# Optimization experiments

Hardware: AMD Instinct MI355X
Metric: run time of the kernel (lower is better)

## Reference

```python
import jax, jax.numpy as jnp
import numpy as np

TOP_K = 4

def setup_inputs() -> dict:
    key = jax.random.key(0)
    ks = jax.random.split(key, 10)
    s = 0.02
    return {
        "x": jax.random.normal(ks[0], (4, 1024, 2048), jnp.float32),
        "expert_bias": jnp.zeros((64,), jnp.float32),
        "router_w": jax.random.normal(ks[1], (64, 2048), jnp.float32) * s,
        "gate_w": jax.random.normal(ks[2], (8192, 2048), jnp.float32) * s,
        "up_w": jax.random.normal(ks[3], (8192, 2048), jnp.float32) * s,
        "down_w": jax.random.normal(ks[4], (2048, 8192), jnp.float32) * s,
        "w_down": jax.random.normal(ks[5], (512, 2048), jnp.float32) * s,
        "w_up": jax.random.normal(ks[6], (2048, 512), jnp.float32) * s,
        "experts_w12": jax.random.normal(ks[7], (64, 512, 2048), jnp.float32) * s,
        "experts_w3": jax.random.normal(ks[8], (64, 1024, 512), jnp.float32) * s,
    }


def reference(x, expert_bias, router_w, gate_w, up_w, down_w, w_down, w_up, experts_w12, experts_w3):
    B, S, D = x.shape
    E = router_w.shape[0]
    K = TOP_K
    h = x.reshape(-1, D)            # [N, D]
    N = h.shape[0]
    NK = N * K

    # --- router (fp32) ---
    logits = h @ router_w.T          # [N, E]
    scores = jax.nn.sigmoid(logits)
    z_loss = jnp.mean(logits * logits) * 1e-4
    sel = scores + expert_bias
    _, topk_idx = jax.lax.top_k(sel, K)                      # [N, K]
    topk_logits = jnp.take_along_axis(logits, topk_idx, axis=1)
    gating = jax.nn.softmax(topk_logits, axis=-1)            # [N, K]

    # --- shared SwiGLU expert ---
    shared = (jax.nn.silu(h @ gate_w.T) * (h @ up_w.T)) @ down_w.T   # [N, D]

    # --- bottleneck down projection ---
    hd = h @ w_down.T                # [N, bottle]
    Bn = hd.shape[1]

    # --- dispatch: sort tokens by expert, capacity max_load per expert ---
    flat = topk_idx.reshape(-1)                      # [NK]
    perm = jnp.argsort(flat)                         # stable sort
    sorted_e = flat[perm]
    counts = jnp.bincount(flat, length=E)
    ptr = jnp.cumsum(counts) - counts                # start offset per expert
    local = jnp.arange(NK) - ptr[sorted_e]           # rank within expert
    max_load = (NK // E // 8 + 6) * 8                # static python int
    num_slots = E * max_load
    mask = local < max_load
    slots = sorted_e * max_load + local
    tok = jnp.repeat(jnp.arange(N), K)               # token id per routed slot

    # reverse_map[slot] = token index (N = dummy)
    rm = jnp.full((num_slots + 1,), N, dtype=jnp.int32)
    rm = rm.at[jnp.where(mask, slots, num_slots)].set(tok[perm].astype(jnp.int32))
    reverse_map = rm[:num_slots]

    hwd = jnp.concatenate([hd, jnp.zeros((1, Bn), hd.dtype)], axis=0)
    padding = hwd[reverse_map].reshape(E, max_load, Bn)

    # --- grouped expert GEMMs ---
    h12 = jnp.einsum('emb,ebf->emf', padding, experts_w12)   # [E, L, 2*F]
    h1, h2 = jnp.split(h12, 2, axis=-1)
    pout = jnp.einsum('emf,efb->emb', jax.nn.silu(h1) * h2, experts_w3)
    pout = pout.reshape(-1, Bn)                              # [num_slots, bottle]

    # --- combine: gather back per (token, k) slot and mix with gating ---
    powd = jnp.concatenate([pout, jnp.zeros((1, Bn), pout.dtype)], axis=0)
    gm = jnp.full((NK + 1,), num_slots, dtype=jnp.int32)
    gm = gm.at[jnp.where(mask, perm, NK)].set(jnp.where(mask, slots, num_slots).astype(jnp.int32))
    gather_map = gm[:NK]
    gathered = powd[gather_map].reshape(N, K, Bn)
    routed_b = jnp.einsum('nk,nkb->nb', gating, gathered)
    routed = routed_b @ w_up.T                               # [N, D]

    # eval mode: route_scale = 1.0, moe_scale = 0.5 (one shared expert), aux_loss = 0
    out = (shared + routed) * 0.5
    return out.reshape(B, S, D), z_loss
```

## Files before the change

### kernel.cpp

```cpp
#include <hip/hip_runtime.h>
#include <math.h>

#define NTOK 4096
#define DMODEL 2048
#define ENUM 64
#define HSH 8192
#define BND 512
#define FEXP 1024
#define MAXL 304
#define EPAD 384
#define ECH 16

typedef float f32x4 __attribute__((ext_vector_type(4)));
using bf16x8 = __attribute__((ext_vector_type(8))) __bf16;

typedef const __attribute__((address_space(1))) unsigned int cgu32;
typedef __attribute__((address_space(3))) unsigned int lu32;
#define GLOAD16(g, l) __builtin_amdgcn_global_load_lds((cgu32*)(g), (lu32*)(l), 16, 0, 0)

__device__ __forceinline__ unsigned short f2bf(float f) {
    union { float f; unsigned int u; } v; v.f = f;
    unsigned int u = v.u;
    return (unsigned short)((u + 0x7FFFu + ((u >> 16) & 1u)) >> 16);
}
__device__ __forceinline__ float bf2f(unsigned short s) {
    union { unsigned int u; float f; } v; v.u = ((unsigned int)s) << 16;
    return v.f;
}

__global__ __launch_bounds__(256) void init_kernel(float* zacc, int* slot2tok, unsigned short* hdz) {
    int i = blockIdx.x * 256 + threadIdx.x;
    if (i == 0) *zacc = 0.f;
    if (i < ENUM * MAXL) slot2tok[i] = NTOK;
    if (i < BND) hdz[i] = 0;
}

__global__ __launch_bounds__(256) void convert_kernel(
    const float* __restrict__ in, unsigned short* __restrict__ out, long long n)
{
    long long stride = (long long)gridDim.x * 256 * 8;
    for (long long i = ((long long)blockIdx.x * 256 + threadIdx.x) * 8; i < n; i += stride) {
        float4 a = *(const float4*)(in + i);
        float4 b = *(const float4*)(in + i + 4);
        union { unsigned short s[8]; uint4 v; } o;
        o.s[0] = f2bf(a.x); o.s[1] = f2bf(a.y); o.s[2] = f2bf(a.z); o.s[3] = f2bf(a.w);
        o.s[4] = f2bf(b.x); o.s[5] = f2bf(b.y); o.s[6] = f2bf(b.z); o.s[7] = f2bf(b.w);
        *(uint4*)(out + i) = o.v;
    }
}

__global__ __launch_bounds__(256) void convert_x_kernel(
    const float* __restrict__ in, unsigned short* __restrict__ hi,
    unsigned short* __restrict__ lo, long long n)
{
    long long stride = (long long)gridDim.x * 256 * 8;
    for (long long i = ((long long)blockIdx.x * 256 + threadIdx.x) * 8; i < n; i += stride) {
        float4 a = *(const float4*)(in + i);
        float4 b = *(const float4*)(in + i + 4);
        union { unsigned short s[8]; uint4 v; } oh, ol;
        float f[8] = {a.x, a.y, a.z, a.w, b.x, b.y, b.z, b.w};
#pragma unroll
        for (int j = 0; j < 8; j++) {
            unsigned short h = f2bf(f[j]);
            oh.s[j] = h;
            ol.s[j] = f2bf(f[j] - bf2f(h));
        }
        *(uint4*)(hi + i) = oh.v;
        *(uint4*)(lo + i) = ol.v;
    }
}

__global__ __launch_bounds__(256) void convert_rw_kernel(
    const float* __restrict__ rw, unsigned short* __restrict__ whi,
    unsigned short* __restrict__ wlo)
{
    int i = (blockIdx.x * 256 + threadIdx.x) * 4;
    if (i >= 128 * 2048) return;
    ushort4 oh = {0, 0, 0, 0}, ol = {0, 0, 0, 0};
    if (i < 64 * 2048) {
        float4 f = *(const float4*)(rw + i);
        float v[4] = {f.x, f.y, f.z, f.w};
        unsigned short h;
        h = f2bf(v[0]); oh.x = h; ol.x = f2bf(v[0] - bf2f(h));
        h = f2bf(v[1]); oh.y = h; ol.y = f2bf(v[1] - bf2f(h));
        h = f2bf(v[2]); oh.z = h; ol.z = f2bf(v[2] - bf2f(h));
        h = f2bf(v[3]); oh.w = h; ol.w = f2bf(v[3] - bf2f(h));
    }
    *(ushort4*)(whi + i) = oh;
    *(ushort4*)(wlo + i) = ol;
}

__global__ __launch_bounds__(256) void tconv_kernel(
    const float* __restrict__ in, unsigned short* __restrict__ out, int Kd, int Nd)
{
    __shared__ float t[32][33];
    size_t zoff = (size_t)blockIdx.z * Kd * Nd;
    in += zoff; out += zoff;
    int n0 = blockIdx.x * 32, k0 = blockIdx.y * 32;
    int r = threadIdx.x >> 3, c = (threadIdx.x & 7) * 4;
    float4 v = *(const float4*)(in + (size_t)(k0 + r) * Nd + n0 + c);
    t[r][c] = v.x; t[r][c + 1] = v.y; t[r][c + 2] = v.z; t[r][c + 3] = v.w;
    __syncthreads();
    ushort4 o;
    o.x = f2bf(t[c + 0][r]); o.y = f2bf(t[c + 1][r]);
    o.z = f2bf(t[c + 2][r]); o.w = f2bf(t[c + 3][r]);
    *(ushort4*)(out + (size_t)(n0 + r) * Kd + k0 + c) = o;
}

__global__ __launch_bounds__(256) void rgemm_kernel(
    const unsigned short* __restrict__ xb, const unsigned short* __restrict__ xlo,
    const unsigned short* __restrict__ whi, const unsigned short* __restrict__ wlo,
    float* __restrict__ logits)
{
    __shared__ unsigned short As[2][128 * 64];
    __shared__ unsigned short Bs[2][128 * 64];
    const int z = blockIdx.z;
    const int m0 = blockIdx.y * 128;
    const int tid = threadIdx.x;
    const int lane = tid & 63;
    const int w = tid >> 6;
    const int wm = (w >> 1) * 64;
    const int wn = (w & 1) * 64;

    const unsigned short* Ab = (z == 2) ? xlo : xb;
    const unsigned short* Bb = (z == 1) ? wlo : whi;
    float* Cb = logits + (size_t)z * NTOK * 128;

    size_t asrc[4], bsrc[4];
    int ldso[4];
#pragma unroll
    for (int i = 0; i < 4; i++) {
        int u = i * 256 + tid;
        int r = u >> 3;
        int ce = ((u & 7) ^ (r & 7)) * 8;
        ldso[i] = u * 8;
        asrc[i] = (size_t)(m0 + r) * DMODEL + ce;
        bsrc[i] = (size_t)r * DMODEL + ce;
    }

    const int lrow = lane & 15;
    const int kg = lane >> 4;
    const int mk = (lrow & 7) << 4;
    int arx[4], brx[4];
#pragma unroll
    for (int t = 0; t < 4; t++) {
        arx[t] = (wm + t * 16 + lrow) * 128;
        brx[t] = (wn + t * 16 + lrow) * 128;
    }

    f32x4 acc[4][4];
#pragma unroll
    for (int a = 0; a < 4; a++)
#pragma unroll
        for (int b = 0; b < 4; b++) acc[a][b] = (f32x4)0.f;

#pragma unroll
    for (int i = 0; i < 4; i++) GLOAD16(Ab + asrc[i], &As[0][ldso[i]]);
#pragma unroll
    for (int i = 0; i < 4; i++) GLOAD16(Bb + bsrc[i], &Bs[0][ldso[i]]);
#pragma unroll
    for (int i = 0; i < 4; i++) GLOAD16(Ab + asrc[i] + 64, &As[1][ldso[i]]);
#pragma unroll
    for (int i = 0; i < 4; i++) GLOAD16(Bb + bsrc[i] + 64, &Bs[1][ldso[i]]);

    const int nt = DMODEL >> 6;
    int cur = 0;
    for (int t = 0; t < nt; ++t) {
        if (t + 1 < nt) asm volatile("s_waitcnt vmcnt(8)" ::: "memory");
        else            asm volatile("s_waitcnt vmcnt(0)" ::: "memory");
        __builtin_amdgcn_s_barrier();
        __builtin_amdgcn_sched_barrier(0);
        const char* Abase = (const char*)&As[cur][0];
        const char* Bbase = (const char*)&Bs[cur][0];
#pragma unroll
        for (int ks = 0; ks < 2; ks++) {
            const int cb = (ks * 64 + kg * 16) ^ mk;
            bf16x8 a[4], b[4];
#pragma unroll
            for (int t2 = 0; t2 < 4; t2++) {
                a[t2] = *(const bf16x8*)(Abase + arx[t2] + cb);
                b[t2] = *(const bf16x8*)(Bbase + brx[t2] + cb);
            }
#pragma unroll
            for (int ni = 0; ni < 4; ni++)
#pragma unroll
                for (int mi = 0; mi < 4; mi++)
                    acc[mi][ni] = __builtin_amdgcn_mfma_f32_16x16x32_bf16(a[mi], b[ni], acc[mi][ni], 0, 0, 0);
        }
        __builtin_amdgcn_sched_barrier(0);
        asm volatile("s_waitcnt lgkmcnt(0)" ::: "memory");
        __builtin_amdgcn_s_barrier();
        __builtin_amdgcn_sched_barrier(0);
        const int kn = (t + 2) * 64;
        if (kn < DMODEL) {
#pragma unroll
            for (int i = 0; i < 4; i++) GLOAD16(Ab + asrc[i] + kn, &As[cur][ldso[i]]);
#pragma unroll
            for (int i = 0; i < 4; i++) GLOAD16(Bb + bsrc[i] + kn, &Bs[cur][ldso[i]]);
        }
        cur ^= 1;
    }

    const int rb0 = m0 + wm + (kg << 2);
#pragma unroll
    for (int mi = 0; mi < 4; mi++)
#pragma unroll
        for (int ni = 0; ni < 4; ni++) {
            int col = wn + ni * 16 + lrow;
#pragma unroll
            for (int r = 0; r < 4; r++)
                Cb[(size_t)(rb0 + mi * 16 + r) * 128 + col] = acc[mi][ni][r];
        }
}

__global__ __launch_bounds__(256) void topk_kernel(
    const float* __restrict__ logits, const float* __restrict__ bias,
    int* __restrict__ topk_idx, float* __restrict__ gating, float* __restrict__ zacc)
{
    __shared__ float zpart[4];
    const size_t Z = (size_t)NTOK * 128;
    int wv = threadIdx.x >> 6, lane = threadIdx.x & 63;
    int n = blockIdx.x * 4 + wv;
    const float* lp = logits + (size_t)n * 128 + lane;
    float logit = lp[0] + lp[Z] + lp[2 * Z];
    float sel = 1.f / (1.f + expf(-logit)) + bias[lane];
    float zsq = logit * logit;
    for (int off = 32; off; off >>= 1) zsq += __shfl_down(zsq, off);
    if (lane == 0) zpart[wv] = zsq;
    __syncthreads();
    if (threadIdx.x == 0) atomicAdd(zacc, zpart[0] + zpart[1] + zpart[2] + zpart[3]);
    float cur = sel;
    float ch_logit[4]; int ch_idx[4];
    for (int kk = 0; kk < 4; kk++) {
        float v = cur; int idx = lane;
        for (int off = 1; off < 64; off <<= 1) {
            float v2 = __shfl_xor(v, off);
            int i2 = __shfl_xor(idx, off);
            if (v2 > v || (v2 == v && i2 < idx)) { v = v2; idx = i2; }
        }
        ch_idx[kk] = idx;
        ch_logit[kk] = __shfl(logit, idx);
        if (lane == idx) cur = -1e30f;
    }
    if (lane == 0) {
        float mx = ch_logit[0];
        for (int kk = 1; kk < 4; kk++) mx = fmaxf(mx, ch_logit[kk]);
        float se = 0.f, ex[4];
        for (int kk = 0; kk < 4; kk++) { ex[kk] = expf(ch_logit[kk] - mx); se += ex[kk]; }
        for (int kk = 0; kk < 4; kk++) {
            topk_idx[n * 4 + kk] = ch_idx[kk];
            gating[n * 4 + kk] = ex[kk] / se;
        }
    }
}

__global__ __launch_bounds__(256) void rank_kernel(
    const int* __restrict__ topk_idx, int* __restrict__ slot2tok, int* __restrict__ gmap)
{
    int e = blockIdx.x;
    __shared__ int wsum[4];
    int tid = threadIdx.x;
    int lane = tid & 63, w = tid >> 6;
    int running = 0;
    for (int c = 0; c < NTOK * 4; c += 256) {
        int i = c + tid;
        int fl = topk_idx[i];
        bool m = (fl == e);
        unsigned long long bal = __ballot(m);
        int prefix = __popcll(bal & ((1ULL << lane) - 1ULL));
        if (lane == 0) wsum[w] = __popcll(bal);
        __syncthreads();
        int wbase = 0;
        for (int j = 0; j < w; j++) wbase += wsum[j];
        int total = wsum[0] + wsum[1] + wsum[2] + wsum[3];
        if (m) {
            int rank = running + wbase + prefix;
            int tok = i >> 2;
            if (rank < MAXL) {
                slot2tok[e * MAXL + rank] = tok;
                gmap[i] = e * MAXL + rank;
            } else gmap[i] = -1;
        }
        running += total;
        __syncthreads();
    }
}

template<int GATHER, int EPI>
__global__ __launch_bounds__(256) void gemm2(
    const unsigned short* __restrict__ A, long long aZ, int lda,
    const int* __restrict__ gtab,
    const unsigned short* __restrict__ Bm, long long bZ, int ldb,
    void* __restrict__ Cb, long long cZ, int ldc,
    int M, int K)
{
    __shared__ unsigned short As[2][128 * 64];
    __shared__ unsigned short Bs[2][128 * 64];
    const int z = blockIdx.z;
    const int m0 = blockIdx.y * 128;
    const int n0 = blockIdx.x * 128;
    const int tid = threadIdx.x;
    const int lane = tid & 63;
    const int w = tid >> 6;
    const int wm = (w >> 1) * 64;
    const int wn = (w & 1) * 64;

    const unsigned short* Ab = A + (GATHER ? (size_t)0 : (size_t)z * aZ);
    const unsigned short* Bb = Bm + (size_t)z * bZ;

    size_t asrc[4], bsrc[4];
    int ldso[4];
#pragma unroll
    for (int i = 0; i < 4; i++) {
        int u = i * 256 + tid;
        int r = u >> 3;
        int ce = ((u & 7) ^ (r & 7)) * 8;
        ldso[i] = u * 8;
        if constexpr (GATHER) {
            int mr = m0 + r;
            int tok = (mr < M) ? gtab[(size_t)z * MAXL + mr] : NTOK;
            asrc[i] = (size_t)tok * lda + ce;
        } else {
            asrc[i] = (size_t)(m0 + r) * lda + ce;
        }
        bsrc[i] = (size_t)(n0 + r) * ldb + ce;
    }

    const int lrow = lane & 15;
    const int kg = lane >> 4;
    const int mk = (lrow & 7) << 4;
    int arx[4], brx[4];
#pragma unroll
    for (int t = 0; t < 4; t++) {
        arx[t] = (wm + t * 16 + lrow) * 128;
        brx[t] = (wn + t * 16 + lrow) * 128;
    }

    f32x4 acc[4][4];
#pragma unroll
    for (int a = 0; a < 4; a++)
#pragma unroll
        for (int b = 0; b < 4; b++) acc[a][b] = (f32x4)0.f;

#pragma unroll
    for (int i = 0; i < 4; i++) GLOAD16(Ab + asrc[i], &As[0][ldso[i]]);
#pragma unroll
    for (int i = 0; i < 4; i++) GLOAD16(Bb + bsrc[i], &Bs[0][ldso[i]]);
    if (64 < K) {
#pragma unroll
        for (int i = 0; i < 4; i++) GLOAD16(Ab + asrc[i] + 64, &As[1][ldso[i]]);
#pragma unroll
        for (int i = 0; i < 4; i++) GLOAD16(Bb + bsrc[i] + 64, &Bs[1][ldso[i]]);
    }

    const int nt = K >> 6;
    int cur = 0;
    for (int t = 0; t < nt; ++t) {
        if (t + 1 < nt) asm volatile("s_waitcnt vmcnt(8)" ::: "memory");
        else            asm volatile("s_waitcnt vmcnt(0)" ::: "memory");
        __builtin_amdgcn_s_barrier();
        __builtin_amdgcn_sched_barrier(0);
        const char* Abase = (const char*)&As[cur][0];
        const char* Bbase = (const char*)&Bs[cur][0];
#pragma unroll
        for (int ks = 0; ks < 2; ks++) {
            const int cb = (ks * 64 + kg * 16) ^ mk;
            bf16x8 a[4], b[4];
#pragma unroll
            for (int t2 = 0; t2 < 4; t2++) {
                a[t2] = *(const bf16x8*)(Abase + arx[t2] + cb);
                b[t2] = *(const bf16x8*)(Bbase + brx[t2] + cb);
            }
#pragma unroll
            for (int ni = 0; ni < 4; ni++)
#pragma unroll
                for (int mi = 0; mi < 4; mi++)
                    acc[mi][ni] = __builtin_amdgcn_mfma_f32_16x16x32_bf16(a[mi], b[ni], acc[mi][ni], 0, 0, 0);
        }
        __builtin_amdgcn_sched_barrier(0);
        asm volatile("s_waitcnt lgkmcnt(0)" ::: "memory");
        __builtin_amdgcn_s_barrier();
        __builtin_amdgcn_sched_barrier(0);
        const int kn = (t + 2) * 64;
        if (kn < K) {
#pragma unroll
            for (int i = 0; i < 4; i++) GLOAD16(Ab + asrc[i] + kn, &As[cur][ldso[i]]);
#pragma unroll
            for (int i = 0; i < 4; i++) GLOAD16(Bb + bsrc[i] + kn, &Bs[cur][ldso[i]]);
        }
        cur ^= 1;
    }

    const int rb0 = m0 + wm + (kg << 2);
#pragma unroll
    for (int mi = 0; mi < 4; mi++)
#pragma unroll
        for (int ni = 0; ni < 4; ni++) {
            int col = n0 + wn + ni * 16 + lrow;
#pragma unroll
            for (int r = 0; r < 4; r++) {
                int row = rb0 + mi * 16 + r;
                if (row < M) {
                    size_t ci = (size_t)z * cZ + (size_t)row * ldc + col;
                    float v = acc[mi][ni][r];
                    if constexpr (EPI == 0) {
                        ((unsigned short*)Cb)[ci] = f2bf(v);
                    } else if constexpr (EPI == 1) {
                        unsigned short* cp = (unsigned short*)Cb + ci;
                        float g = bf2f(*cp);
                        *cp = f2bf(g / (1.f + expf(-g)) * v);
                    } else if constexpr (EPI == 2) {
                        ((float*)Cb)[ci] = v;
                    } else {
                        float* cp = (float*)Cb + ci;
                        *cp = (*cp + v) * 0.5f;
                    }
                }
            }
        }
}

template<int DUAL>
__global__ __launch_bounds__(512) void gemm6(
    const unsigned short* __restrict__ A, int lda,
    const unsigned short* __restrict__ B1, const unsigned short* __restrict__ B2, int ldb,
    void* __restrict__ Cb, int ldc, int ncol0, int K)
{
    constexpr int RING = DUAL ? 3 : 4;
    __shared__ unsigned short As[RING * 128 * 32];
    __shared__ unsigned short B1s[RING * 256 * 32];
    __shared__ unsigned short B2s[DUAL ? RING * 256 * 32 : 64];
    const int m0 = blockIdx.y * 128;
    const int n0 = blockIdx.x * 256;
    const int tid = threadIdx.x;
    const int lane = tid & 63;
    const int w = tid >> 6;
    const int wm = (w >> 2) * 64;
    const int wn = (w & 3) * 64;

    size_t asrc;
    int ldsoA;
    {
        int r = tid >> 2;
        int ce = ((tid & 3) ^ ((r >> 1) & 3)) * 8;
        ldsoA = tid * 8;
        asrc = (size_t)(m0 + r) * lda + ce;
    }
    size_t bsrc[2];
    int ldsoB[2];
#pragma unroll
    for (int i = 0; i < 2; i++) {
        int u = i * 512 + tid;
        int r = u >> 2;
        int ce = ((u & 3) ^ ((r >> 1) & 3)) * 8;
        ldsoB[i] = u * 8;
        bsrc[i] = (size_t)(n0 + r) * ldb + ce;
    }

    const int lrow = lane & 15;
    const int kg = lane >> 4;
    const int un = (kg ^ ((lrow >> 1) & 3)) << 4;
    int arx[4], brx[4];
#pragma unroll
    for (int mi = 0; mi < 4; mi++) arx[mi] = (wm + mi * 16 + lrow) * 64 + un;
#pragma unroll
    for (int ni = 0; ni < 4; ni++) brx[ni] = (wn + ni * 16 + lrow) * 64 + un;

    f32x4 acc1[4][4];
    f32x4 acc2[DUAL ? 4 : 1][DUAL ? 4 : 1];
#pragma unroll
    for (int a = 0; a < 4; a++)
#pragma unroll
        for (int b = 0; b < 4; b++) {
            acc1[a][b] = (f32x4)0.f;
            if constexpr (DUAL) acc2[a][b] = (f32x4)0.f;
        }

    const int NT = K >> 5;
    const int PRO = DUAL ? 2 : 3;
    for (int t = 0; t < PRO && t < NT; ++t) {
        const int kn = t * 32;
        unsigned short* as = &As[(t % RING) * 128 * 32];
        unsigned short* b1s = &B1s[(t % RING) * 256 * 32];
        GLOAD16(A + asrc + kn, &as[ldsoA]);
        GLOAD16(B1 + bsrc[0] + kn, &b1s[ldsoB[0]]);
        GLOAD16(B1 + bsrc[1] + kn, &b1s[ldsoB[1]]);
        if constexpr (DUAL) {
            unsigned short* b2s = &B2s[(t % RING) * 256 * 32];
            GLOAD16(B2 + bsrc[0] + kn, &b2s[ldsoB[0]]);
            GLOAD16(B2 + bsrc[1] + kn, &b2s[ldsoB[1]]);
        }
    }

    for (int kt = 0; kt < NT; ++kt) {
        if constexpr (DUAL) {
            if (kt + 1 < NT) asm volatile("s_waitcnt vmcnt(5)" ::: "memory");
            else             asm volatile("s_waitcnt vmcnt(0)" ::: "memory");
        } else {
            if (kt + 2 < NT)       asm volatile("s_waitcnt vmcnt(6)" ::: "memory");
            else if (kt + 1 < NT)  asm volatile("s_waitcnt vmcnt(3)" ::: "memory");
            else                   asm volatile("s_waitcnt vmcnt(0)" ::: "memory");
        }
        __builtin_amdgcn_s_barrier();
        __builtin_amdgcn_sched_barrier(0);

        const int slot = kt % RING;
        const char* Ab = (const char*)&As[slot * 128 * 32];
        const char* Bb1 = (const char*)&B1s[slot * 256 * 32];
        const char* Bb2 = DUAL ? (const char*)&B2s[slot * 256 * 32] : nullptr;

        const int tstage = kt + (DUAL ? 2 : 3);
        const bool pf = (tstage < NT);
        const int sslot = tstage % RING;
        const int kn = tstage * 32;
        unsigned short* sas = &As[sslot * 128 * 32];
        unsigned short* sb1 = &B1s[sslot * 256 * 32];
        unsigned short* sb2 = DUAL ? &B2s[sslot * 256 * 32] : nullptr;

        bf16x8 b1[4], b2[DUAL ? 4 : 1];
#pragma unroll
        for (int ni = 0; ni < 4; ni++) {
            b1[ni] = *(const bf16x8*)(Bb1 + brx[ni]);
            if constexpr (DUAL) b2[ni] = *(const bf16x8*)(Bb2 + brx[ni]);
        }

#define G6_PHASE(q, GL)                                                              \
        {                                                                            \
            bf16x8 af = *(const bf16x8*)(Ab + arx[q]);                               \
            GL;                                                                      \
            __builtin_amdgcn_s_setprio(1);                                           \
            _Pragma("unroll")                                                        \
            for (int ni = 0; ni < 4; ni++) {                                         \
                acc1[q][ni] = __builtin_amdgcn_mfma_f32_16x16x32_bf16(               \
                    af, b1[ni], acc1[q][ni], 0, 0, 0);                               \
                if constexpr (DUAL)                                                  \
                    acc2[q][ni] = __builtin_amdgcn_mfma_f32_16x16x32_bf16(           \
                        af, b2[ni], acc2[q][ni], 0, 0, 0);                           \
            }                                                                        \
            __builtin_amdgcn_s_setprio(0);                                           \
            __builtin_amdgcn_sched_barrier(0);                                       \
        }

        G6_PHASE(0, if (pf) GLOAD16(A + asrc + kn, &sas[ldsoA]))
        G6_PHASE(1, if (pf) GLOAD16(B1 + bsrc[0] + kn, &sb1[ldsoB[0]]))
        G6_PHASE(2, if (pf) { GLOAD16(B1 + bsrc[1] + kn, &sb1[ldsoB[1]]);
                              if constexpr (DUAL) GLOAD16(B2 + bsrc[0] + kn, &sb2[ldsoB[0]]); })
        G6_PHASE(3, if (pf) { if constexpr (DUAL) GLOAD16(B2 + bsrc[1] + kn, &sb2[ldsoB[1]]); })
#undef G6_PHASE
    }

    const int rb0 = m0 + wm + (kg << 2);
#pragma unroll
    for (int mi = 0; mi < 4; mi++)
#pragma unroll
        for (int ni = 0; ni < 4; ni++) {
            int col = ncol0 + n0 + wn + ni * 16 + lrow;
#pragma unroll
            for (int r = 0; r < 4; r++) {
                int row = rb0 + mi * 16 + r;
                if constexpr (DUAL) {
                    float g = acc1[mi][ni][r];
                    float u = acc2[mi][ni][r];
                    ((unsigned short*)Cb)[(size_t)row * ldc + col] =
                        f2bf(g / (1.f + expf(-g)) * u);
                } else {
                    ((float*)Cb)[(size_t)row * ldc + col] = acc1[mi][ni][r];
                }
            }
        }
}

template<int EPI>
__global__ __launch_bounds__(512) void gemm7(
    const unsigned short* __restrict__ A, int lda,
    const unsigned short* __restrict__ Bm, int ldb,
    unsigned short* __restrict__ C, int ldc, int K)
{
    __shared__ unsigned short As[2][256 * 64];
    __shared__ unsigned short Bs[2][256 * 64];
    const int m0 = blockIdx.y * 256;
    const int n0 = blockIdx.x * 256;
    const int tid = threadIdx.x;
    const int lane = tid & 63;
    const int w = tid >> 6;
    const int wm = (w >> 2) * 128;
    const int wn = (w & 3) * 64;

    size_t asrc[4], bsrc[4];
    int ldso[4];
#pragma unroll
    for (int i = 0; i < 4; i++) {
        int u = i * 512 + tid;
        int r = u >> 3;
        int ce = ((u & 7) ^ (r & 7)) * 8;
        ldso[i] = u * 8;
        asrc[i] = (size_t)(m0 + r) * lda + ce;
        bsrc[i] = (size_t)(n0 + r) * ldb + ce;
    }

    const int lrow = lane & 15;
    const int kg = lane >> 4;
    const int mk = (lrow & 7) << 4;
    int arx[8], brx[4];
#pragma unroll
    for (int mi = 0; mi < 8; mi++) arx[mi] = (wm + mi * 16 + lrow) * 128;
#pragma unroll
    for (int ni = 0; ni < 4; ni++) brx[ni] = (wn + ni * 16 + lrow) * 128;

    f32x4 acc[8][4];
#pragma unroll
    for (int a = 0; a < 8; a++)
#pragma unroll
        for (int b = 0; b < 4; b++) acc[a][b] = (f32x4)0.f;

#pragma unroll
    for (int i = 0; i < 4; i++) GLOAD16(A + asrc[i], &As[0][ldso[i]]);
#pragma unroll
    for (int i = 0; i < 4; i++) GLOAD16(Bm + bsrc[i], &Bs[0][ldso[i]]);

    const int NT = K >> 6;
    for (int t = 0; t < NT; ++t) {
        asm volatile("s_waitcnt vmcnt(0)" ::: "memory");
        __builtin_amdgcn_s_barrier();
        __builtin_amdgcn_sched_barrier(0);

        const char* Ab = (const char*)&As[t & 1][0];
        const char* Bb = (const char*)&Bs[t & 1][0];
        const bool pf = (t + 1 < NT);
        const int nb = (t + 1) & 1;
        const int kn = (t + 1) * 64;
        const int cb0 = (kg * 16) ^ mk;
        const int cb1 = (64 + kg * 16) ^ mk;

        bf16x8 b0[4], b1v[4];
        bf16x8 af[4];

#define G7_PHASE(MH, KS, CB, READB, GL0, GL1)                                        \
        {                                                                            \
            if constexpr (READB) {                                                   \
                _Pragma("unroll")                                                    \
                for (int ni = 0; ni < 4; ni++)                                       \
                    ((KS) ? b1v : b0)[ni] = *(const bf16x8*)(Bb + brx[ni] + (CB));   \
            }                                                                        \
            _Pragma("unroll")                                                        \
            for (int mi = 0; mi < 4; mi++)                                           \
                af[mi] = *(const bf16x8*)(Ab + arx[(MH) * 4 + mi] + (CB));           \
            if (pf) { GL0; GL1; }                                                    \
            __builtin_amdgcn_s_barrier();                                            \
            asm volatile("s_waitcnt lgkmcnt(0)" ::: "memory");                       \
            __builtin_amdgcn_sched_barrier(0);                                       \
            __builtin_amdgcn_s_setprio(1);                                           \
            _Pragma("unroll")                                                        \
            for (int ni = 0; ni < 4; ni++)                                           \
                _Pragma("unroll")                                                    \
                for (int mi = 0; mi < 4; mi++)                                       \
                    acc[(MH) * 4 + mi][ni] = __builtin_amdgcn_mfma_f32_16x16x32_bf16(\
                        af[mi], ((KS) ? b1v : b0)[ni], acc[(MH) * 4 + mi][ni], 0, 0, 0);\
            __builtin_amdgcn_s_setprio(0);                                           \
            __builtin_amdgcn_sched_barrier(0);                                       \
            __builtin_amdgcn_s_barrier();                                            \
        }

        G7_PHASE(0, 0, cb0, true,
                 GLOAD16(A + asrc[0] + kn, &As[nb][ldso[0]]),
                 GLOAD16(A + asrc[1] + kn, &As[nb][ldso[1]]))
        G7_PHASE(1, 0, cb0, false,
                 GLOAD16(A + asrc[2] + kn, &As[nb][ldso[2]]),
                 GLOAD16(A + asrc[3] + kn, &As[nb][ldso[3]]))
        G7_PHASE(0, 1, cb1, true,
                 GLOAD16(Bm + bsrc[0] + kn, &Bs[nb][ldso[0]]),
                 GLOAD16(Bm + bsrc[1] + kn, &Bs[nb][ldso[1]]))
        G7_PHASE(1, 1, cb1, false,
                 GLOAD16(Bm + bsrc[2] + kn, &Bs[nb][ldso[2]]),
                 GLOAD16(Bm + bsrc[3] + kn, &Bs[nb][ldso[3]]))
#undef G7_PHASE
    }

    const int rb0 = m0 + wm + (kg << 2);
#pragma unroll
    for (int mi = 0; mi < 8; mi++)
#pragma unroll
        for (int ni = 0; ni < 4; ni++) {
            int col = n0 + wn + ni * 16 + lrow;
#pragma unroll
            for (int r = 0; r < 4; r++) {
                int row = rb0 + mi * 16 + r;
                size_t ci = (size_t)row * ldc + col;
                float v = acc[mi][ni][r];
                if constexpr (EPI == 0) {
                    C[ci] = f2bf(v);
                } else {
                    unsigned short* cp = C + ci;
                    float g = bf2f(*cp);
                    *cp = f2bf(g / (1.f + expf(-g)) * v);
                }
            }
        }
}

__global__ __launch_bounds__(256) void siluact_kernel(
    const unsigned short* __restrict__ h12, unsigned short* __restrict__ act)
{
    int e = blockIdx.y, m = blockIdx.x;
    const unsigned short* hr = h12 + ((size_t)e * EPAD + m) * 2048;
    unsigned short* ar = act + ((size_t)e * EPAD + m) * 1024;
    int j = threadIdx.x * 4;
    ushort4 h1 = *(const ushort4*)(hr + j);
    ushort4 h2 = *(const ushort4*)(hr + 1024 + j);
    ushort4 o;
    float v;
    v = bf2f(h1.x); o.x = f2bf(v / (1.f + expf(-v)) * bf2f(h2.x));
    v = bf2f(h1.y); o.y = f2bf(v / (1.f + expf(-v)) * bf2f(h2.y));
    v = bf2f(h1.z); o.z = f2bf(v / (1.f + expf(-v)) * bf2f(h2.z));
    v = bf2f(h1.w); o.w = f2bf(v / (1.f + expf(-v)) * bf2f(h2.w));
    *(ushort4*)(ar + j) = o;
}

__global__ __launch_bounds__(256) void gather_kernel(
    const unsigned short* __restrict__ pout, const int* __restrict__ gmap,
    const float* __restrict__ gating, unsigned short* __restrict__ routed_b)
{
    int n = blockIdx.x;
    int j = threadIdx.x * 2;
    float a0 = 0.f, a1 = 0.f;
#pragma unroll
    for (int kk = 0; kk < 4; kk++) {
        int slot = gmap[n * 4 + kk];
        float g = gating[n * 4 + kk];
        if (slot >= 0) {
            const unsigned short* pr = pout + (size_t)slot * BND + j;
            a0 += g * bf2f(pr[0]);
            a1 += g * bf2f(pr[1]);
        }
    }
    routed_b[(size_t)n * BND + j] = f2bf(a0);
    routed_b[(size_t)n * BND + j + 1] = f2bf(a1);
}

__global__ void zloss_kernel(const float* zacc, float* out) {
    out[0] = zacc[0] * (1.0e-4f / (float)(NTOK * ENUM));
}

extern "C" void kernel_launch(void* const* d_in, const int* in_sizes, int n_in,
                              void* d_out, int out_size, void* d_ws, size_t ws_size,
                              hipStream_t stream)
{
    const float* x      = (const float*)d_in[0];
    const float* ebias  = (const float*)d_in[1];
    const float* rw     = (const float*)d_in[2];
    const float* gate_w = (const float*)d_in[3];
    const float* up_w   = (const float*)d_in[4];
    const float* down_w = (const float*)d_in[5];
    const float* w_down = (const float*)d_in[6];
    const float* w_up   = (const float*)d_in[7];
    const float* w12    = (const float*)d_in[8];
    const float* w3     = (const float*)d_in[9];
    float* out = (float*)d_out;

    char* ws = (char*)d_ws;
    size_t off = 0;
    auto alloc = [&](size_t b) { size_t o = off; off += (b + 255) & ~(size_t)255; return o; };
    float* zacc     = (float*)(ws + alloc(4));
    int*   topk     = (int*)(ws + alloc((size_t)NTOK * 4 * 4));
    float* gating   = (float*)(ws + alloc((size_t)NTOK * 4 * 4));
    int*   gmap     = (int*)(ws + alloc((size_t)NTOK * 4 * 4));
    int*   slot2tok = (int*)(ws + alloc((size_t)ENUM * MAXL * 4));
    unsigned short* xb     = (unsigned short*)(ws + alloc((size_t)NTOK * DMODEL * 2));
    unsigned short* hd     = (unsigned short*)(ws + alloc((size_t)(NTOK + 1) * BND * 2));
    unsigned short* rb     = (unsigned short*)(ws + alloc((size_t)NTOK * BND * 2));
    unsigned short* wdownb = (unsigned short*)(ws + alloc((size_t)BND * DMODEL * 2));
    unsigned short* wupb   = (unsigned short*)(ws + alloc((size_t)DMODEL * BND * 2));
    unsigned short* wbuf   = (unsigned short*)(ws + alloc((size_t)HSH * DMODEL * 2));
    unsigned short* H1     = (unsigned short*)(ws + alloc((size_t)NTOK * HSH * 2));
    unsigned short* h12  = H1;
    unsigned short* act  = H1 + (size_t)ECH * EPAD * 2048;
    unsigned short* pout = H1 + (size_t)ECH * EPAD * 2048 + (size_t)ECH * EPAD * 1024;
    unsigned short* xlo    = H1;
    float*          logits = (float*)((char*)H1 + (size_t)NTOK * DMODEL * 2);
    unsigned short* whi    = (unsigned short*)((char*)logits + (size_t)3 * NTOK * 128 * 4);
    unsigned short* wlo    = whi + (size_t)128 * DMODEL;

    init_kernel<<<(ENUM * MAXL + 255) / 256, 256, 0, stream>>>(zacc, slot2tok, hd + (size_t)NTOK * BND);

    convert_x_kernel<<<1024, 256, 0, stream>>>(x, xb, xlo, (long long)NTOK * DMODEL);
    convert_rw_kernel<<<(128 * 2048 / 4 + 255) / 256, 256, 0, stream>>>(rw, whi, wlo);
    rgemm_kernel<<<dim3(1, NTOK / 128, 3), 256, 0, stream>>>(xb, xlo, whi, wlo, logits);
    topk_kernel<<<NTOK / 4, 256, 0, stream>>>(logits, ebias, topk, gating, zacc);
    rank_kernel<<<ENUM, 256, 0, stream>>>(topk, slot2tok, gmap);

    convert_kernel<<<256, 256, 0, stream>>>(w_down, wdownb, (long long)BND * DMODEL);
    convert_kernel<<<256, 256, 0, stream>>>(w_up, wupb, (long long)DMODEL * BND);

    gemm2<0, 0><<<dim3(BND / 128, NTOK / 128, 1), 256, 0, stream>>>(
        xb, 0, DMODEL, nullptr, wdownb, 0, DMODEL, hd, 0, BND, NTOK, DMODEL);

    convert_kernel<<<1024, 256, 0, stream>>>(gate_w, wbuf, (long long)HSH * DMODEL);
    gemm7<0><<<dim3(HSH / 256, NTOK / 256), 512, 0, stream>>>(
        xb, DMODEL, wbuf, DMODEL, H1, HSH, DMODEL);
    convert_kernel<<<1024, 256, 0, stream>>>(up_w, wbuf, (long long)HSH * DMODEL);
    gemm7<1><<<dim3(HSH / 256, NTOK / 256), 512, 0, stream>>>(
        xb, DMODEL, wbuf, DMODEL, H1, HSH, DMODEL);
    convert_kernel<<<1024, 256, 0, stream>>>(down_w, wbuf, (long long)DMODEL * HSH);
    gemm6<0><<<dim3(DMODEL / 256, NTOK / 128), 512, 0, stream>>>(
        H1, HSH, wbuf, nullptr, HSH, out, DMODEL, 0, HSH);

    for (int c = 0; c < ENUM / ECH; c++) {
        tconv_kernel<<<dim3(2048 / 32, 512 / 32, ECH), 256, 0, stream>>>(
            w12 + (size_t)c * ECH * 512 * 2048, wbuf, 512, 2048);
        gemm2<1, 0><<<dim3(2048 / 128, 3, ECH), 256, 0, stream>>>(
            hd, 0, BND, slot2tok + (size_t)c * ECH * MAXL,
            wbuf, (long long)2048 * 512, 512,
            h12, (long long)EPAD * 2048, 2048, MAXL, BND);
        tconv_kernel<<<dim3(512 / 32, 1024 / 32, ECH), 256, 0, stream>>>(
            w3 + (size_t)c * ECH * 1024 * 512, wbuf, 1024, 512);
        siluact_kernel<<<dim3(EPAD, ECH), 256, 0, stream>>>(h12, act);
        gemm2<0, 0><<<dim3(BND / 128, 3, ECH), 256, 0, stream>>>(
            act, (long long)EPAD * FEXP, FEXP, nullptr,
            wbuf, (long long)BND * FEXP, FEXP,
            pout + (size_t)c * ECH * MAXL * BND, (long long)MAXL * BND, BND, MAXL, FEXP);
    }

    gather_kernel<<<NTOK, 256, 0, stream>>>(pout, gmap, gating, rb);

    gemm2<0, 3><<<dim3(DMODEL / 128, NTOK / 128, 1), 256, 0, stream>>>(
        rb, 0, BND, nullptr, wupb, 0, BND, out, 0, DMODEL, NTOK, BND);

    zloss_kernel<<<1, 1, 0, stream>>>(zacc, out + (size_t)NTOK * DMODEL);
}
```

Baseline: 1.101 ms.

## Replace gemm7 with 4-stage pipelined gemm4 and fuse w_down GEMM into gate GEMM

Replaces the double-buffered BK=64 gemm7 with a gemm4 kernel that uses a 4-slot ring of BK=32 tiles, partial vmcnt waits, and one barrier per k-step instead of several per phase. The gate-projection launch also takes extra column blocks that compute the bottleneck down projection (x @ w_down^T into hd), so the separate gemm2 launch is removed. The aim is to hide global-load latency, cut synchronisation overhead and save a launch, at the cost of a new swizzle layout and a heavier-tail grid for the fused launch.

```diff
diff --git a/kernel.cpp b/kernel.cpp
--- a/kernel.cpp
+++ b/kernel.cpp
@@ -420,6 +420,128 @@
         }
 }
 
+template<int EPI>
+__global__ __launch_bounds__(512) void gemm4(
+    const unsigned short* __restrict__ A, int lda,
+    const unsigned short* __restrict__ B1, int ldb,
+    unsigned short* __restrict__ C1, int ldc1,
+    const unsigned short* __restrict__ B2,
+    unsigned short* __restrict__ C2, int ldc2,
+    int nMainX, int K)
+{
+    __shared__ unsigned short As[4][256 * 32];
+    __shared__ unsigned short Bs[4][256 * 32];
+    const unsigned short* Bm;
+    unsigned short* C;
+    int ldc, n0;
+    if ((int)blockIdx.x < nMainX) { Bm = B1; C = C1; ldc = ldc1; n0 = blockIdx.x * 256; }
+    else { Bm = B2; C = C2; ldc = ldc2; n0 = (blockIdx.x - nMainX) * 256; }
+    const int m0 = blockIdx.y * 256;
+    const int tid = threadIdx.x;
+    const int lane = tid & 63;
+    const int w = tid >> 6;
+    const int wm = (w >> 2) * 128;
+    const int wn = (w & 3) * 64;
+
+    size_t asrc[2], bsrc[2];
+    int ldso[2];
+#pragma unroll
+    for (int i = 0; i < 2; i++) {
+        int u = i * 512 + tid;
+        int r = u >> 2;
+        int ce = ((u & 3) ^ ((r >> 1) & 3)) * 8;
+        ldso[i] = u * 8;
+        asrc[i] = (size_t)(m0 + r) * lda + ce;
+        bsrc[i] = (size_t)(n0 + r) * ldb + ce;
+    }
+
+    const int lrow = lane & 15;
+    const int kg = lane >> 4;
+    const int un = (kg ^ ((lrow >> 1) & 3)) << 4;
+    int arx[8], brx[4];
+#pragma unroll
+    for (int mi = 0; mi < 8; mi++) arx[mi] = (wm + mi * 16 + lrow) * 64 + un;
+#pragma unroll
+    for (int ni = 0; ni < 4; ni++) brx[ni] = (wn + ni * 16 + lrow) * 64 + un;
+
+    f32x4 acc[8][4];
+#pragma unroll
+    for (int a = 0; a < 8; a++)
+#pragma unroll
+        for (int b = 0; b < 4; b++) acc[a][b] = (f32x4)0.f;
+
+    const int NT = K >> 5;
+    for (int t = 0; t < 3 && t < NT; ++t) {
+        const int kn = t * 32;
+        GLOAD16(A + asrc[0] + kn, &As[t][ldso[0]]);
+        GLOAD16(A + asrc[1] + kn, &As[t][ldso[1]]);
+        GLOAD16(Bm + bsrc[0] + kn, &Bs[t][ldso[0]]);
+        GLOAD16(Bm + bsrc[1] + kn, &Bs[t][ldso[1]]);
+    }
+
+    for (int kt = 0; kt < NT; ++kt) {
+        if (kt < NT - 2)       asm volatile("s_waitcnt vmcnt(8)" ::: "memory");
+        else if (kt == NT - 2) asm volatile("s_waitcnt vmcnt(4)" ::: "memory");
+        else                   asm volatile("s_waitcnt vmcnt(0)" ::: "memory");
+        __builtin_amdgcn_s_barrier();
+        __builtin_amdgcn_sched_barrier(0);
+
+        const char* Ab = (const char*)&As[kt & 3][0];
+        const char* Bb = (const char*)&Bs[kt & 3][0];
+        const bool pf = (kt + 3 < NT);
+        const int slot = (kt + 3) & 3;
+        const int kn = (kt + 3) * 32;
+
+        bf16x8 b[4];
+#pragma unroll
+        for (int ni = 0; ni < 4; ni++) b[ni] = *(const bf16x8*)(Bb + brx[ni]);
+
+#define G4_PHASE(q, GL)                                                              \
+        {                                                                            \
+            bf16x8 a0 = *(const bf16x8*)(Ab + arx[2 * (q)]);                         \
+            bf16x8 a1 = *(const bf16x8*)(Ab + arx[2 * (q) + 1]);                     \
+            GL;                                                                      \
+            __builtin_amdgcn_s_setprio(1);                                           \
+            _Pragma("unroll")                                                        \
+            for (int ni = 0; ni < 4; ni++) {                                         \
+                acc[2 * (q)][ni] = __builtin_amdgcn_mfma_f32_16x16x32_bf16(          \
+                    a0, b[ni], acc[2 * (q)][ni], 0, 0, 0);                           \
+                acc[2 * (q) + 1][ni] = __builtin_amdgcn_mfma_f32_16x16x32_bf16(      \
+                    a1, b[ni], acc[2 * (q) + 1][ni], 0, 0, 0);                       \
+            }                                                                        \
+            __builtin_amdgcn_s_setprio(0);                                           \
+            __builtin_amdgcn_sched_barrier(0);                                       \
+        }
+
+        G4_PHASE(0, if (pf) GLOAD16(A + asrc[0] + kn, &As[slot][ldso[0]]))
+        G4_PHASE(1, if (pf) GLOAD16(A + asrc[1] + kn, &As[slot][ldso[1]]))
+        G4_PHASE(2, if (pf) GLOAD16(Bm + bsrc[0] + kn, &Bs[slot][ldso[0]]))
+        G4_PHASE(3, if (pf) GLOAD16(Bm + bsrc[1] + kn, &Bs[slot][ldso[1]]))
+#undef G4_PHASE
+    }
+
+    const int rb0 = m0 + wm + (kg << 2);
+#pragma unroll
+    for (int mi = 0; mi < 8; mi++)
+#pragma unroll
+        for (int ni = 0; ni < 4; ni++) {
+            int col = n0 + wn + ni * 16 + lrow;
+#pragma unroll
+            for (int r = 0; r < 4; r++) {
+                int row = rb0 + mi * 16 + r;
+                size_t ci = (size_t)row * ldc + col;
+                float v = acc[mi][ni][r];
+                if constexpr (EPI == 0) {
+                    C[ci] = f2bf(v);
+                } else {
+                    unsigned short* cp = C + ci;
+                    float g = bf2f(*cp);
+                    *cp = f2bf(g / (1.f + expf(-g)) * v);
+                }
+            }
+        }
+}
+
 template<int DUAL>
 __global__ __launch_bounds__(512) void gemm6(
     const unsigned short* __restrict__ A, int lda,
@@ -565,134 +687,6 @@
                         f2bf(g / (1.f + expf(-g)) * u);
                 } else {
                     ((float*)Cb)[(size_t)row * ldc + col] = acc1[mi][ni][r];
-                }
-            }
-        }
-}
-
-template<int EPI>
-__global__ __launch_bounds__(512) void gemm7(
-    const unsigned short* __restrict__ A, int lda,
-    const unsigned short* __restrict__ Bm, int ldb,
-    unsigned short* __restrict__ C, int ldc, int K)
-{
-    __shared__ unsigned short As[2][256 * 64];
-    __shared__ unsigned short Bs[2][256 * 64];
-    const int m0 = blockIdx.y * 256;
-    const int n0 = blockIdx.x * 256;
-    const int tid = threadIdx.x;
-    const int lane = tid & 63;
-    const int w = tid >> 6;
-    const int wm = (w >> 2) * 128;
-    const int wn = (w & 3) * 64;
-
-    size_t asrc[4], bsrc[4];
-    int ldso[4];
-#pragma unroll
-    for (int i = 0; i < 4; i++) {
-        int u = i * 512 + tid;
-        int r = u >> 3;
-        int ce = ((u & 7) ^ (r & 7)) * 8;
-        ldso[i] = u * 8;
-        asrc[i] = (size_t)(m0 + r) * lda + ce;
-        bsrc[i] = (size_t)(n0 + r) * ldb + ce;
-    }
-
-    const int lrow = lane & 15;
-    const int kg = lane >> 4;
-    const int mk = (lrow & 7) << 4;
-    int arx[8], brx[4];
-#pragma unroll
-    for (int mi = 0; mi < 8; mi++) arx[mi] = (wm + mi * 16 + lrow) * 128;
-#pragma unroll
-    for (int ni = 0; ni < 4; ni++) brx[ni] = (wn + ni * 16 + lrow) * 128;
-
-    f32x4 acc[8][4];
-#pragma unroll
-    for (int a = 0; a < 8; a++)
-#pragma unroll
-        for (int b = 0; b < 4; b++) acc[a][b] = (f32x4)0.f;
-
-#pragma unroll
-    for (int i = 0; i < 4; i++) GLOAD16(A + asrc[i], &As[0][ldso[i]]);
-#pragma unroll
-    for (int i = 0; i < 4; i++) GLOAD16(Bm + bsrc[i], &Bs[0][ldso[i]]);
-
-    const int NT = K >> 6;
-    for (int t = 0; t < NT; ++t) {
-        asm volatile("s_waitcnt vmcnt(0)" ::: "memory");
-        __builtin_amdgcn_s_barrier();
-        __builtin_amdgcn_sched_barrier(0);
-
-        const char* Ab = (const char*)&As[t & 1][0];
-        const char* Bb = (const char*)&Bs[t & 1][0];
-        const bool pf = (t + 1 < NT);
-        const int nb = (t + 1) & 1;
-        const int kn = (t + 1) * 64;
-        const int cb0 = (kg * 16) ^ mk;
-        const int cb1 = (64 + kg * 16) ^ mk;
-
-        bf16x8 b0[4], b1v[4];
-        bf16x8 af[4];
-
-#define G7_PHASE(MH, KS, CB, READB, GL0, GL1)                                        \
-        {                                                                            \
-            if constexpr (READB) {                                                   \
-                _Pragma("unroll")                                                    \
-                for (int ni = 0; ni < 4; ni++)                                       \
-                    ((KS) ? b1v : b0)[ni] = *(const bf16x8*)(Bb + brx[ni] + (CB));   \
-            }                                                                        \
-            _Pragma("unroll")                                                        \
-            for (int mi = 0; mi < 4; mi++)                                           \
-                af[mi] = *(const bf16x8*)(Ab + arx[(MH) * 4 + mi] + (CB));           \
-            if (pf) { GL0; GL1; }                                                    \
-            __builtin_amdgcn_s_barrier();                                            \
-            asm volatile("s_waitcnt lgkmcnt(0)" ::: "memory");                       \
-            __builtin_amdgcn_sched_barrier(0);                                       \
-            __builtin_amdgcn_s_setprio(1);                                           \
-            _Pragma("unroll")                                                        \
-            for (int ni = 0; ni < 4; ni++)                                           \
-                _Pragma("unroll")                                                    \
-                for (int mi = 0; mi < 4; mi++)                                       \
-                    acc[(MH) * 4 + mi][ni] = __builtin_amdgcn_mfma_f32_16x16x32_bf16(\
-                        af[mi], ((KS) ? b1v : b0)[ni], acc[(MH) * 4 + mi][ni], 0, 0, 0);\
-            __builtin_amdgcn_s_setprio(0);                                           \
-            __builtin_amdgcn_sched_barrier(0);                                       \
-            __builtin_amdgcn_s_barrier();                                            \
-        }
-
-        G7_PHASE(0, 0, cb0, true,
-                 GLOAD16(A + asrc[0] + kn, &As[nb][ldso[0]]),
-                 GLOAD16(A + asrc[1] + kn, &As[nb][ldso[1]]))
-        G7_PHASE(1, 0, cb0, false,
-                 GLOAD16(A + asrc[2] + kn, &As[nb][ldso[2]]),
-                 GLOAD16(A + asrc[3] + kn, &As[nb][ldso[3]]))
-        G7_PHASE(0, 1, cb1, true,
-                 GLOAD16(Bm + bsrc[0] + kn, &Bs[nb][ldso[0]]),
-                 GLOAD16(Bm + bsrc[1] + kn, &Bs[nb][ldso[1]]))
-        G7_PHASE(1, 1, cb1, false,
-                 GLOAD16(Bm + bsrc[2] + kn, &Bs[nb][ldso[2]]),
-                 GLOAD16(Bm + bsrc[3] + kn, &Bs[nb][ldso[3]]))
-#undef G7_PHASE
-    }
-
-    const int rb0 = m0 + wm + (kg << 2);
-#pragma unroll
-    for (int mi = 0; mi < 8; mi++)
-#pragma unroll
-        for (int ni = 0; ni < 4; ni++) {
-            int col = n0 + wn + ni * 16 + lrow;
-#pragma unroll
-            for (int r = 0; r < 4; r++) {
-                int row = rb0 + mi * 16 + r;
-                size_t ci = (size_t)row * ldc + col;
-                float v = acc[mi][ni][r];
-                if constexpr (EPI == 0) {
-                    C[ci] = f2bf(v);
-                } else {
-                    unsigned short* cp = C + ci;
-                    float g = bf2f(*cp);
-                    *cp = f2bf(g / (1.f + expf(-g)) * v);
                 }
             }
         }
@@ -791,15 +785,12 @@
     convert_kernel<<<256, 256, 0, stream>>>(w_down, wdownb, (long long)BND * DMODEL);
     convert_kernel<<<256, 256, 0, stream>>>(w_up, wupb, (long long)DMODEL * BND);
 
-    gemm2<0, 0><<<dim3(BND / 128, NTOK / 128, 1), 256, 0, stream>>>(
-        xb, 0, DMODEL, nullptr, wdownb, 0, DMODEL, hd, 0, BND, NTOK, DMODEL);
-
     convert_kernel<<<1024, 256, 0, stream>>>(gate_w, wbuf, (long long)HSH * DMODEL);
-    gemm7<0><<<dim3(HSH / 256, NTOK / 256), 512, 0, stream>>>(
-        xb, DMODEL, wbuf, DMODEL, H1, HSH, DMODEL);
+    gemm4<0><<<dim3(HSH / 256 + BND / 256, NTOK / 256), 512, 0, stream>>>(
+        xb, DMODEL, wbuf, DMODEL, H1, HSH, wdownb, hd, BND, HSH / 256, DMODEL);
     convert_kernel<<<1024, 256, 0, stream>>>(up_w, wbuf, (long long)HSH * DMODEL);
-    gemm7<1><<<dim3(HSH / 256, NTOK / 256), 512, 0, stream>>>(
-        xb, DMODEL, wbuf, DMODEL, H1, HSH, DMODEL);
+    gemm4<1><<<dim3(HSH / 256, NTOK / 256), 512, 0, stream>>>(
+        xb, DMODEL, wbuf, DMODEL, H1, HSH, nullptr, nullptr, 0, HSH / 256, DMODEL);
     convert_kernel<<<1024, 256, 0, stream>>>(down_w, wbuf, (long long)DMODEL * HSH);
     gemm6<0><<<dim3(DMODEL / 256, NTOK / 128), 512, 0, stream>>>(
         H1, HSH, wbuf, nullptr, HSH, out, DMODEL, 0, HSH);
```

New measurement: 1.143 ms. 1.04x slower.
